# Kernel tuning notes

Hardware: AMD Instinct MI355X
Metric: run time of the kernel (lower is better)

Reference implementation:

```python
import jax, jax.numpy as jnp
import numpy as np

B, A, C, H, W = 4, 5, 64, 128, 128


def _base_grid(h, w):
    # torch F.affine_grid with align_corners=False: pixel-center normalized coords
    xs = (2.0 * jnp.arange(w, dtype=jnp.float32) + 1.0) / w - 1.0
    ys = (2.0 * jnp.arange(h, dtype=jnp.float32) + 1.0) / h - 1.0
    X, Y = jnp.meshgrid(xs, ys)  # [h,w]
    return jnp.stack([X, Y, jnp.ones_like(X)], axis=-1)  # [h,w,3]


def _grid_sample(img, grid):
    # img [C,H,W]; grid [H,W,2] = (x,y) normalized; bilinear, zeros padding, align_corners=False
    c, h, w = img.shape
    ix = ((grid[..., 0] + 1.0) * w - 1.0) * 0.5
    iy = ((grid[..., 1] + 1.0) * h - 1.0) * 0.5
    ix0 = jnp.floor(ix); iy0 = jnp.floor(iy)
    ix1 = ix0 + 1.0; iy1 = iy0 + 1.0
    wx1 = ix - ix0; wy1 = iy - iy0
    wx0 = 1.0 - wx1; wy0 = 1.0 - wy1

    def gather(iyf, ixf):
        valid = (iyf >= 0) & (iyf <= h - 1) & (ixf >= 0) & (ixf <= w - 1)
        iyc = jnp.clip(iyf.astype(jnp.int32), 0, h - 1)
        ixc = jnp.clip(ixf.astype(jnp.int32), 0, w - 1)
        return img[:, iyc, ixc] * valid[None].astype(img.dtype)  # [C,H,W]

    return (gather(iy0, ix0) * (wy0 * wx0)[None]
            + gather(iy0, ix1) * (wy0 * wx1)[None]
            + gather(iy1, ix0) * (wy1 * wx0)[None]
            + gather(iy1, ix1) * (wy1 * wx1)[None])


_sample_batch = jax.vmap(_grid_sample)


def setup_inputs() -> dict:
    key = jax.random.key(0)
    k1, k2, k3 = jax.random.split(key, 3)
    feats = jax.random.normal(k1, (B, A, C, H, W), dtype=jnp.float32)
    trans_matrices = jax.random.normal(k2, (B, A, A, 4, 4), dtype=jnp.float32)
    num_agent_tensor = jax.random.randint(k3, (B, A), 1, A + 1, dtype=jnp.int64)
    return {"feats": feats, "trans_matrices": trans_matrices,
            "num_agent_tensor": num_agent_tensor}


def reference(feats, trans_matrices, num_agent_tensor):
    b, a, c, h, w = feats.shape
    T = trans_matrices  # [B,A(target i),A(neighbor j),4,4]
    zeros = jnp.zeros(T.shape[:3], T.dtype)
    ones = jnp.ones_like(zeros)
    # theta_rot = [[T00, T01, 0], [T10, T11, 0]]
    theta_rot = jnp.stack([
        jnp.stack([T[..., 0, 0], T[..., 0, 1], zeros], axis=-1),
        jnp.stack([T[..., 1, 0], T[..., 1, 1], zeros], axis=-1)], axis=-2)
    x_t = 4.0 * T[..., 0, 3] / 128.0
    y_t = -(4.0 * T[..., 1, 3]) / 128.0
    theta_trans = jnp.stack([
        jnp.stack([ones, zeros, x_t], axis=-1),
        jnp.stack([zeros, ones, y_t], axis=-1)], axis=-2)
    base = _base_grid(h, w)  # [H,W,3]
    grid_rot = jnp.einsum('hwk,bijrk->bijhwr', base, theta_rot)
    grid_trans = jnp.einsum('hwk,bijrk->bijhwr', base, theta_trans)
    n = b * a * a
    # neighbor feature feats[b, j] broadcast over target index i
    feats_nb = jnp.broadcast_to(feats[:, None], (b, a, a, c, h, w)).reshape(n, c, h, w)
    w1 = _sample_batch(feats_nb, grid_rot.reshape(n, h, w, 2))
    w2 = _sample_batch(w1, grid_trans.reshape(n, h, w, 2)).reshape(b, a, a, c, h, w)
    na = num_agent_tensor[:, 0]  # [B]
    ar = jnp.arange(a)
    valid = ((ar[None, :, None] < na[:, None, None])
             & (ar[None, None, :] < na[:, None, None])
             & (ar[:, None] != ar[None, :])[None])  # [B,A_i,A_j]
    fused = feats + jnp.sum(w2 * valid[..., None, None, None].astype(feats.dtype), axis=2)
    # agents2batch: concatenate per-agent slices along batch dim -> [A*B, C, H, W]
    return fused.transpose(1, 0, 2, 3, 4).reshape(a * b, c, h, w)
```

## Files before the change

kernel.cpp:

```cpp
#include <hip/hip_runtime.h>


typedef float floatv4 __attribute__((ext_vector_type(4)));

constexpr int Bc = 4, Ac = 5, Cc = 64, Hc = 128, Wc = 128;
constexpr int HWc = Hc * Wc;
constexpr int NP  = Bc * Ac;
constexpr int NG  = Cc / 4;
constexpr int GPB = 4;
constexpr int TW = 64, TH = 4;
constexpr int WW = TW + 1, WSZ = WW * (TH + 1);
constexpr size_t WS_NEED = (size_t)NP * Cc * HWc * sizeof(float);

__global__ __launch_bounds__(256)
void fafmimo_repack(const float* __restrict__ feats, float4* __restrict__ ws)
{
    const int idx  = (int)(blockIdx.x * 256 + threadIdx.x);
    const int pix4 = (idx & 4095) * 4;
    const int t    = idx >> 12;
    const int g    = t & 15;
    const int p    = t >> 4;
    const floatv4* s =
        (const floatv4*)(feats + ((size_t)p * Cc + g * 4) * HWc + pix4);
    const floatv4 r0 = __builtin_nontemporal_load(s);
    const floatv4 r1 = __builtin_nontemporal_load(s + HWc / 4);
    const floatv4 r2 = __builtin_nontemporal_load(s + 2 * (HWc / 4));
    const floatv4 r3 = __builtin_nontemporal_load(s + 3 * (HWc / 4));
    float4* d = ws + ((size_t)p * NG + g) * HWc + pix4;
    d[0] = make_float4(r0.x, r1.x, r2.x, r3.x);
    d[1] = make_float4(r0.y, r1.y, r2.y, r3.y);
    d[2] = make_float4(r0.z, r1.z, r2.z, r3.z);
    d[3] = make_float4(r0.w, r1.w, r2.w, r3.w);
}

__global__ __launch_bounds__(256)
void fafmimo_main(const float4* __restrict__ ws,
                  const float* __restrict__ trans,
                  const int*   __restrict__ num_agent,
                  float*       __restrict__ out)
{
    __shared__ float4 w1s[GPB][WSZ];

    const int z  = (int)blockIdx.z;
    const int bi = z % NP;
    const int q  = z / NP;
    const int g0 = q * GPB;
    const int b  = bi / Ac;
    const int i  = bi - b * Ac;
    const int tx = (int)threadIdx.x, ty = (int)threadIdx.y;
    const int tid = ty * TW + tx;
    const int x0 = (int)blockIdx.x * TW, y0 = (int)blockIdx.y * TH;
    const int x  = x0 + tx, y = y0 + ty;
    const int pix = y * Wc + x;
    const int na = num_agent[b * Ac];

    const float xv  = (2.0f * (float)x  + 1.0f) / 128.0f - 1.0f;
    const float yv  = (2.0f * (float)y  + 1.0f) / 128.0f - 1.0f;
    const float xv0 = (2.0f * (float)x0 + 1.0f) / 128.0f - 1.0f;
    const float yv0 = (2.0f * (float)y0 + 1.0f) / 128.0f - 1.0f;

    float4 acc[GPB];
    #pragma unroll
    for (int cg = 0; cg < GPB; ++cg)
        acc[cg] = ws[((size_t)bi * NG + g0 + cg) * HWc + pix];

    if (i < na) {
        for (int j = 0; j < Ac; ++j) {
            if (j == i || j >= na) continue;

            const float* Tm = trans + (size_t)((b * Ac + i) * Ac + j) * 16;
            const float r00 = Tm[0], r01 = Tm[1], t03 = Tm[3];
            const float r10 = Tm[4], r11 = Tm[5], t13 = Tm[7];
            const float x_t =  (4.0f * t03) / 128.0f;
            const float y_t = -(4.0f * t13) / 128.0f;

            const int fdx = (int)floorf(((xv0 + x_t + 1.0f) * 128.0f - 1.0f) * 0.5f) - x0;
            const int fdy = (int)floorf(((yv0 + y_t + 1.0f) * 128.0f - 1.0f) * 0.5f) - y0;

            const float4* __restrict__ pj0 = ws + ((size_t)((b * Ac + j) * NG) + g0) * HWc;
            const float4* __restrict__ pj1 = pj0 + HWc;
            const float4* __restrict__ pj2 = pj0 + 2 * HWc;
            const float4* __restrict__ pj3 = pj0 + 3 * HWc;

            for (int e = tid; e < WSZ; e += TW * TH) {
                const int ry = e / WW, rx = e - ry * WW;
                const int jy = y0 + fdy + ry, jx = x0 + fdx + rx;
                const int jyc = min(max(jy, 0), 127);
                const int jxc = min(max(jx, 0), 127);

                const float Xs = (2.0f * (float)jxc + 1.0f) / 128.0f - 1.0f;
                const float Ys = (2.0f * (float)jyc + 1.0f) / 128.0f - 1.0f;
                const float gx = Xs * r00 + Ys * r01;
                const float gy = Xs * r10 + Ys * r11;
                const float ixs = ((gx + 1.0f) * 128.0f - 1.0f) * 0.5f;
                const float iys = ((gy + 1.0f) * 128.0f - 1.0f) * 0.5f;
                const float sx0 = floorf(ixs), sy0 = floorf(iys);
                const float u1 = ixs - sx0, v1 = iys - sy0;
                const float u0 = 1.0f - u1, v0 = 1.0f - v1;

                const bool xin = (sx0 >= 0.0f) & (sx0 <= 126.0f);
                const float a  = xin ? u0 : ((sx0 == -1.0f)  ? u1 : 0.0f);
                const float bb = xin ? u1 : ((sx0 == 127.0f) ? u0 : 0.0f);
                const int xb = min(max((int)sx0, 0), 126);

                const bool vr0 = (sy0 >= 0.0f) & (sy0 <= 127.0f);
                const bool vr1 = (sy0 >= -1.0f) & (sy0 <= 126.0f);
                const float wr0 = v0 * (vr0 ? 1.0f : 0.0f);
                const float wr1 = v1 * (vr1 ? 1.0f : 0.0f);
                const int o0 = min(max((int)sy0, 0), 127) * Wc + xb;
                const int o1 = min(max((int)sy0 + 1, 0), 127) * Wc + xb;

                #pragma unroll
                for (int cg = 0; cg < GPB; ++cg) {
                    const float4* __restrict__ pg =
                        (cg == 0) ? pj0 : (cg == 1) ? pj1 : (cg == 2) ? pj2 : pj3;
                    const float4 t0a = pg[o0], t0b = pg[o0 + 1];
                    const float4 t1a = pg[o1], t1b = pg[o1 + 1];
                    float4 w1;
                    w1.x = wr0 * fmaf(a, t0a.x, bb * t0b.x) + wr1 * fmaf(a, t1a.x, bb * t1b.x);
                    w1.y = wr0 * fmaf(a, t0a.y, bb * t0b.y) + wr1 * fmaf(a, t1a.y, bb * t1b.y);
                    w1.z = wr0 * fmaf(a, t0a.z, bb * t0b.z) + wr1 * fmaf(a, t1a.z, bb * t1b.z);
                    w1.w = wr0 * fmaf(a, t0a.w, bb * t0b.w) + wr1 * fmaf(a, t1a.w, bb * t1b.w);
                    w1s[cg][e] = w1;
                }
            }
            __syncthreads();

            const float ix2 = ((xv + x_t + 1.0f) * 128.0f - 1.0f) * 0.5f;
            const float iy2 = ((yv + y_t + 1.0f) * 128.0f - 1.0f) * 0.5f;
            const int jx0 = x + fdx, jy0 = y + fdy;
            const float fx1 = ix2 - (float)jx0, fx0 = 1.0f - fx1;
            const float fy1 = iy2 - (float)jy0, fy0 = 1.0f - fy1;
            const float vx0 = (jx0 >= 0 && jx0 <= 127) ? 1.0f : 0.0f;
            const float vx1 = (jx0 >= -1 && jx0 <= 126) ? 1.0f : 0.0f;
            const float vy0 = (jy0 >= 0 && jy0 <= 127) ? 1.0f : 0.0f;
            const float vy1 = (jy0 >= -1 && jy0 <= 126) ? 1.0f : 0.0f;
            const float w00 = fy0 * vy0 * fx0 * vx0;
            const float w01 = fy0 * vy0 * fx1 * vx1;
            const float w10 = fy1 * vy1 * fx0 * vx0;
            const float w11 = fy1 * vy1 * fx1 * vx1;

            const int base = ty * WW + tx;
            #pragma unroll
            for (int cg = 0; cg < GPB; ++cg) {
                const float4 s00 = w1s[cg][base],      s01 = w1s[cg][base + 1];
                const float4 s10 = w1s[cg][base + WW], s11 = w1s[cg][base + WW + 1];
                acc[cg].x += w00 * s00.x + w01 * s01.x + w10 * s10.x + w11 * s11.x;
                acc[cg].y += w00 * s00.y + w01 * s01.y + w10 * s10.y + w11 * s11.y;
                acc[cg].z += w00 * s00.z + w01 * s01.z + w10 * s10.z + w11 * s11.z;
                acc[cg].w += w00 * s00.w + w01 * s01.w + w10 * s10.w + w11 * s11.w;
            }
            __syncthreads();
        }
    }

    #pragma unroll
    for (int cg = 0; cg < GPB; ++cg) {
        float* __restrict__ ob =
            out + ((size_t)(i * Bc + b) * Cc + (g0 + cg) * 4) * HWc + pix;
        __builtin_nontemporal_store(acc[cg].x, ob);
        __builtin_nontemporal_store(acc[cg].y, ob + HWc);
        __builtin_nontemporal_store(acc[cg].z, ob + 2 * HWc);
        __builtin_nontemporal_store(acc[cg].w, ob + 3 * HWc);
    }
}

constexpr int CHK = 16;
__global__ __launch_bounds__(256)
void fafmimo_direct(const float* __restrict__ feats,
                    const float* __restrict__ trans,
                    const int*   __restrict__ num_agent,
                    float*       __restrict__ out)
{
    const int z  = (int)blockIdx.z;
    const int bi = z % NP;
    const int c0 = (z / NP) * CHK;
    const int b  = bi / Ac;
    const int i  = bi - b * Ac;
    const int x  = (int)(blockIdx.x * 64 + threadIdx.x);
    const int y  = (int)(blockIdx.y * 4  + threadIdx.y);
    const int pix = y * Wc + x;
    const int na = num_agent[b * Ac];

    const float xv = (2.0f * (float)x + 1.0f) / 128.0f - 1.0f;
    const float yv = (2.0f * (float)y + 1.0f) / 128.0f - 1.0f;

    const float* __restrict__ fi =
        feats + (size_t)(b * Ac + i) * Cc * HWc + (size_t)c0 * HWc;
    float* __restrict__ ob =
        out + (size_t)(i * Bc + b) * Cc * HWc + (size_t)c0 * HWc;

    float acc[CHK];
    #pragma unroll
    for (int k = 0; k < CHK; ++k) acc[k] = fi[k * HWc + pix];

    if (i < na) {
        for (int j = 0; j < Ac; ++j) {
            if (j == i || j >= na) continue;
            const float* Tm = trans + (size_t)((b * Ac + i) * Ac + j) * 16;
            const float r00 = Tm[0], r01 = Tm[1], t03 = Tm[3];
            const float r10 = Tm[4], r11 = Tm[5], t13 = Tm[7];
            const float x_t =  (4.0f * t03) / 128.0f;
            const float y_t = -(4.0f * t13) / 128.0f;
            const float ix2 = ((xv + x_t + 1.0f) * 128.0f - 1.0f) * 0.5f;
            const float iy2 = ((yv + y_t + 1.0f) * 128.0f - 1.0f) * 0.5f;
            const float fx0 = floorf(ix2), fy0 = floorf(iy2);
            const float wx1 = ix2 - fx0,   wy1 = iy2 - fy0;
            const float wx0 = 1.0f - wx1,  wy0 = 1.0f - wy1;

            int off[8]; float wA[8], wB[8];
            #pragma unroll
            for (int cy = 0; cy < 2; ++cy) {
                #pragma unroll
                for (int cx = 0; cx < 2; ++cx) {
                    const float jyf = fy0 + (float)cy;
                    const float jxf = fx0 + (float)cx;
                    const bool v2 = (jyf >= 0.0f) & (jyf <= 127.0f)
                                  & (jxf >= 0.0f) & (jxf <= 127.0f);
                    const float w2 = (cy ? wy1 : wy0) * (cx ? wx1 : wx0)
                                   * (v2 ? 1.0f : 0.0f);
                    const int jy = min(max((int)jyf, 0), 127);
                    const int jx = min(max((int)jxf, 0), 127);
                    const float Xs = (2.0f * (float)jx + 1.0f) / 128.0f - 1.0f;
                    const float Ys = (2.0f * (float)jy + 1.0f) / 128.0f - 1.0f;
                    const float gx = Xs * r00 + Ys * r01;
                    const float gy = Xs * r10 + Ys * r11;
                    const float ixs = ((gx + 1.0f) * 128.0f - 1.0f) * 0.5f;
                    const float iys = ((gy + 1.0f) * 128.0f - 1.0f) * 0.5f;
                    const float sx0 = floorf(ixs), sy0 = floorf(iys);
                    const float u1 = ixs - sx0, v1 = iys - sy0;
                    const float u0 = 1.0f - u1,  v0f = 1.0f - v1;
                    const bool xin = (sx0 >= 0.0f) & (sx0 <= 126.0f);
                    const float a  = xin ? u0 : ((sx0 == -1.0f)  ? u1 : 0.0f);
                    const float bbp = xin ? u1 : ((sx0 == 127.0f) ? u0 : 0.0f);
                    const int xb = min(max((int)sx0, 0), 126);
                    const int e = (cy * 2 + cx) * 2;
                    #pragma unroll
                    for (int r = 0; r < 2; ++r) {
                        const float syr = sy0 + (float)r;
                        const bool vy = (syr >= 0.0f) & (syr <= 127.0f);
                        const float wyr = (r ? v1 : v0f) * (vy ? 1.0f : 0.0f) * w2;
                        const int syc = min(max((int)syr, 0), 127);
                        off[e + r] = syc * Wc + xb;
                        wA[e + r]  = wyr * a;
                        wB[e + r]  = wyr * bbp;
                    }
                }
            }

            const float* __restrict__ fj =
                feats + (size_t)(b * Ac + j) * Cc * HWc + (size_t)c0 * HWc;
            #pragma unroll 4
            for (int k = 0; k < CHK; ++k) {
                const float* __restrict__ p = fj + (size_t)k * HWc;
                float s0 = 0.0f, s1 = 0.0f;
                #pragma unroll
                for (int r = 0; r < 8; ++r) {
                    s0 = fmaf(wA[r], p[off[r]],     s0);
                    s1 = fmaf(wB[r], p[off[r] + 1], s1);
                }
                acc[k] += s0 + s1;
            }
        }
    }

    #pragma unroll
    for (int k = 0; k < CHK; ++k)
        __builtin_nontemporal_store(acc[k], &ob[k * HWc + pix]);
}

extern "C" void kernel_launch(void* const* d_in, const int* in_sizes, int n_in,
                              void* d_out, int out_size, void* d_ws, size_t ws_size,
                              hipStream_t stream) {
    const float* feats     = (const float*)d_in[0];
    const float* trans     = (const float*)d_in[1];
    const int*   num_agent = (const int*)d_in[2];
    float* out = (float*)d_out;

    if (ws_size >= WS_NEED) {
        float4* ws = (float4*)d_ws;
        hipLaunchKernelGGL(fafmimo_repack, dim3(NP * NG * (HWc / 4) / 256),
                           dim3(256), 0, stream, feats, ws);
        dim3 grid(Wc / TW, Hc / TH, NP * (NG / GPB));
        dim3 block(TW, TH, 1);
        hipLaunchKernelGGL(fafmimo_main, grid, block, 0, stream,
                           ws, trans, num_agent, out);
    } else {
        dim3 grid(Wc / 64, Hc / 4, NP * 4);
        dim3 block(64, 4, 1);
        hipLaunchKernelGGL(fafmimo_direct, grid, block, 0, stream,
                           feats, trans, num_agent, out);
    }
}
```

Baseline: 226.2 us.

## Double-buffer shared warp tile across neighbors and halve channel groups per block

Restructures the per-neighbor loop into a double-buffered pipeline. While one shared-memory buffer is being consumed by the second bilinear stencil, the next neighbor's first-stage sample is written into the other buffer, so only one barrier per iteration is needed instead of two. Channel groups per block drop from 4 to 2, which doubles the grid and keeps the shared footprint the same. In exchange, the rotation-stage index math and the trans loads are redone for every block at twice the count, and occupancy depends on the register pressure of the overlapped fill and stencil.

```diff
diff --git a/kernel.cpp b/kernel.cpp
--- a/kernel.cpp
+++ b/kernel.cpp
@@ -7,7 +7,8 @@
 constexpr int HWc = Hc * Wc;
 constexpr int NP  = Bc * Ac;
 constexpr int NG  = Cc / 4;
-constexpr int GPB = 4;
+constexpr int GPB = 2;
+constexpr int NQ  = NG / GPB;
 constexpr int TW = 64, TH = 4;
 constexpr int WW = TW + 1, WSZ = WW * (TH + 1);
 constexpr size_t WS_NEED = (size_t)NP * Cc * HWc * sizeof(float);
@@ -39,12 +40,11 @@
                   const int*   __restrict__ num_agent,
                   float*       __restrict__ out)
 {
-    __shared__ float4 w1s[GPB][WSZ];
+    __shared__ float4 w1s[2][GPB][WSZ];
 
     const int z  = (int)blockIdx.z;
     const int bi = z % NP;
-    const int q  = z / NP;
-    const int g0 = q * GPB;
+    const int g0 = (z / NP) * GPB;
     const int b  = bi / Ac;
     const int i  = bi - b * Ac;
     const int tx = (int)threadIdx.x, ty = (int)threadIdx.y;
@@ -64,93 +64,114 @@
     for (int cg = 0; cg < GPB; ++cg)
         acc[cg] = ws[((size_t)bi * NG + g0 + cg) * HWc + pix];
 
-    if (i < na) {
-        for (int j = 0; j < Ac; ++j) {
-            if (j == i || j >= na) continue;
-
-            const float* Tm = trans + (size_t)((b * Ac + i) * Ac + j) * 16;
-            const float r00 = Tm[0], r01 = Tm[1], t03 = Tm[3];
-            const float r10 = Tm[4], r11 = Tm[5], t13 = Tm[7];
-            const float x_t =  (4.0f * t03) / 128.0f;
-            const float y_t = -(4.0f * t13) / 128.0f;
-
-            const int fdx = (int)floorf(((xv0 + x_t + 1.0f) * 128.0f - 1.0f) * 0.5f) - x0;
-            const int fdy = (int)floorf(((yv0 + y_t + 1.0f) * 128.0f - 1.0f) * 0.5f) - y0;
-
-            const float4* __restrict__ pj0 = ws + ((size_t)((b * Ac + j) * NG) + g0) * HWc;
-            const float4* __restrict__ pj1 = pj0 + HWc;
-            const float4* __restrict__ pj2 = pj0 + 2 * HWc;
-            const float4* __restrict__ pj3 = pj0 + 3 * HWc;
-
-            for (int e = tid; e < WSZ; e += TW * TH) {
-                const int ry = e / WW, rx = e - ry * WW;
-                const int jy = y0 + fdy + ry, jx = x0 + fdx + rx;
-                const int jyc = min(max(jy, 0), 127);
-                const int jxc = min(max(jx, 0), 127);
-
-                const float Xs = (2.0f * (float)jxc + 1.0f) / 128.0f - 1.0f;
-                const float Ys = (2.0f * (float)jyc + 1.0f) / 128.0f - 1.0f;
-                const float gx = Xs * r00 + Ys * r01;
-                const float gy = Xs * r10 + Ys * r11;
-                const float ixs = ((gx + 1.0f) * 128.0f - 1.0f) * 0.5f;
-                const float iys = ((gy + 1.0f) * 128.0f - 1.0f) * 0.5f;
-                const float sx0 = floorf(ixs), sy0 = floorf(iys);
-                const float u1 = ixs - sx0, v1 = iys - sy0;
-                const float u0 = 1.0f - u1, v0 = 1.0f - v1;
-
-                const bool xin = (sx0 >= 0.0f) & (sx0 <= 126.0f);
-                const float a  = xin ? u0 : ((sx0 == -1.0f)  ? u1 : 0.0f);
-                const float bb = xin ? u1 : ((sx0 == 127.0f) ? u0 : 0.0f);
-                const int xb = min(max((int)sx0, 0), 126);
-
-                const bool vr0 = (sy0 >= 0.0f) & (sy0 <= 127.0f);
-                const bool vr1 = (sy0 >= -1.0f) & (sy0 <= 126.0f);
-                const float wr0 = v0 * (vr0 ? 1.0f : 0.0f);
-                const float wr1 = v1 * (vr1 ? 1.0f : 0.0f);
-                const int o0 = min(max((int)sy0, 0), 127) * Wc + xb;
-                const int o1 = min(max((int)sy0 + 1, 0), 127) * Wc + xb;
-
-                #pragma unroll
-                for (int cg = 0; cg < GPB; ++cg) {
-                    const float4* __restrict__ pg =
-                        (cg == 0) ? pj0 : (cg == 1) ? pj1 : (cg == 2) ? pj2 : pj3;
-                    const float4 t0a = pg[o0], t0b = pg[o0 + 1];
-                    const float4 t1a = pg[o1], t1b = pg[o1 + 1];
-                    float4 w1;
-                    w1.x = wr0 * fmaf(a, t0a.x, bb * t0b.x) + wr1 * fmaf(a, t1a.x, bb * t1b.x);
-                    w1.y = wr0 * fmaf(a, t0a.y, bb * t0b.y) + wr1 * fmaf(a, t1a.y, bb * t1b.y);
-                    w1.z = wr0 * fmaf(a, t0a.z, bb * t0b.z) + wr1 * fmaf(a, t1a.z, bb * t1b.z);
-                    w1.w = wr0 * fmaf(a, t0a.w, bb * t0b.w) + wr1 * fmaf(a, t1a.w, bb * t1b.w);
-                    w1s[cg][e] = w1;
-                }
-            }
-            __syncthreads();
-
-            const float ix2 = ((xv + x_t + 1.0f) * 128.0f - 1.0f) * 0.5f;
-            const float iy2 = ((yv + y_t + 1.0f) * 128.0f - 1.0f) * 0.5f;
-            const int jx0 = x + fdx, jy0 = y + fdy;
-            const float fx1 = ix2 - (float)jx0, fx0 = 1.0f - fx1;
-            const float fy1 = iy2 - (float)jy0, fy0 = 1.0f - fy1;
-            const float vx0 = (jx0 >= 0 && jx0 <= 127) ? 1.0f : 0.0f;
-            const float vx1 = (jx0 >= -1 && jx0 <= 126) ? 1.0f : 0.0f;
-            const float vy0 = (jy0 >= 0 && jy0 <= 127) ? 1.0f : 0.0f;
-            const float vy1 = (jy0 >= -1 && jy0 <= 126) ? 1.0f : 0.0f;
-            const float w00 = fy0 * vy0 * fx0 * vx0;
-            const float w01 = fy0 * vy0 * fx1 * vx1;
-            const float w10 = fy1 * vy1 * fx0 * vx0;
-            const float w11 = fy1 * vy1 * fx1 * vx1;
-
-            const int base = ty * WW + tx;
+    auto nextj = [&](int jp) {
+        for (int j = jp + 1; j < na; ++j)
+            if (j != i) return j;
+        return Ac;
+    };
+
+    auto fill = [&](int buf, int j) {
+        const float* Tm = trans + (size_t)((b * Ac + i) * Ac + j) * 16;
+        const float r00 = Tm[0], r01 = Tm[1], t03 = Tm[3];
+        const float r10 = Tm[4], r11 = Tm[5], t13 = Tm[7];
+        const float x_t =  (4.0f * t03) / 128.0f;
+        const float y_t = -(4.0f * t13) / 128.0f;
+        const int fdx = (int)floorf(((xv0 + x_t + 1.0f) * 128.0f - 1.0f) * 0.5f) - x0;
+        const int fdy = (int)floorf(((yv0 + y_t + 1.0f) * 128.0f - 1.0f) * 0.5f) - y0;
+        const float4* __restrict__ pj0 =
+            ws + ((size_t)((b * Ac + j) * NG) + g0) * HWc;
+        const float4* __restrict__ pj1 = pj0 + HWc;
+
+        for (int e = tid; e < WSZ; e += TW * TH) {
+            const int ry = e / WW, rx = e - ry * WW;
+            const int jy = y0 + fdy + ry, jx = x0 + fdx + rx;
+            const int jyc = min(max(jy, 0), 127);
+            const int jxc = min(max(jx, 0), 127);
+
+            const float Xs = (2.0f * (float)jxc + 1.0f) / 128.0f - 1.0f;
+            const float Ys = (2.0f * (float)jyc + 1.0f) / 128.0f - 1.0f;
+            const float gx = Xs * r00 + Ys * r01;
+            const float gy = Xs * r10 + Ys * r11;
+            const float ixs = ((gx + 1.0f) * 128.0f - 1.0f) * 0.5f;
+            const float iys = ((gy + 1.0f) * 128.0f - 1.0f) * 0.5f;
+            const float sx0 = floorf(ixs), sy0 = floorf(iys);
+            const float u1 = ixs - sx0, v1 = iys - sy0;
+            const float u0 = 1.0f - u1, v0 = 1.0f - v1;
+
+            const bool xin = (sx0 >= 0.0f) & (sx0 <= 126.0f);
+            const float a  = xin ? u0 : ((sx0 == -1.0f)  ? u1 : 0.0f);
+            const float bb = xin ? u1 : ((sx0 == 127.0f) ? u0 : 0.0f);
+            const int xb = min(max((int)sx0, 0), 126);
+
+            const bool vr0 = (sy0 >= 0.0f) & (sy0 <= 127.0f);
+            const bool vr1 = (sy0 >= -1.0f) & (sy0 <= 126.0f);
+            const float wr0 = v0 * (vr0 ? 1.0f : 0.0f);
+            const float wr1 = v1 * (vr1 ? 1.0f : 0.0f);
+            const int o0 = min(max((int)sy0, 0), 127) * Wc + xb;
+            const int o1 = min(max((int)sy0 + 1, 0), 127) * Wc + xb;
+
             #pragma unroll
             for (int cg = 0; cg < GPB; ++cg) {
-                const float4 s00 = w1s[cg][base],      s01 = w1s[cg][base + 1];
-                const float4 s10 = w1s[cg][base + WW], s11 = w1s[cg][base + WW + 1];
-                acc[cg].x += w00 * s00.x + w01 * s01.x + w10 * s10.x + w11 * s11.x;
-                acc[cg].y += w00 * s00.y + w01 * s01.y + w10 * s10.y + w11 * s11.y;
-                acc[cg].z += w00 * s00.z + w01 * s01.z + w10 * s10.z + w11 * s11.z;
-                acc[cg].w += w00 * s00.w + w01 * s01.w + w10 * s10.w + w11 * s11.w;
+                const float4* __restrict__ pg = (cg == 0) ? pj0 : pj1;
+                const float4 t0a = pg[o0], t0b = pg[o0 + 1];
+                const float4 t1a = pg[o1], t1b = pg[o1 + 1];
+                float4 w1;
+                w1.x = wr0 * fmaf(a, t0a.x, bb * t0b.x) + wr1 * fmaf(a, t1a.x, bb * t1b.x);
+                w1.y = wr0 * fmaf(a, t0a.y, bb * t0b.y) + wr1 * fmaf(a, t1a.y, bb * t1b.y);
+                w1.z = wr0 * fmaf(a, t0a.z, bb * t0b.z) + wr1 * fmaf(a, t1a.z, bb * t1b.z);
+                w1.w = wr0 * fmaf(a, t0a.w, bb * t0b.w) + wr1 * fmaf(a, t1a.w, bb * t1b.w);
+                w1s[buf][cg][e] = w1;
             }
-            __syncthreads();
+        }
+    };
+
+    auto stencil = [&](int buf, int j) {
+        const float* Tm = trans + (size_t)((b * Ac + i) * Ac + j) * 16;
+        const float t03 = Tm[3], t13 = Tm[7];
+        const float x_t =  (4.0f * t03) / 128.0f;
+        const float y_t = -(4.0f * t13) / 128.0f;
+        const int fdx = (int)floorf(((xv0 + x_t + 1.0f) * 128.0f - 1.0f) * 0.5f) - x0;
+        const int fdy = (int)floorf(((yv0 + y_t + 1.0f) * 128.0f - 1.0f) * 0.5f) - y0;
+
+        const float ix2 = ((xv + x_t + 1.0f) * 128.0f - 1.0f) * 0.5f;
+        const float iy2 = ((yv + y_t + 1.0f) * 128.0f - 1.0f) * 0.5f;
+        const int jx0 = x + fdx, jy0 = y + fdy;
+        const float fx1 = ix2 - (float)jx0, fx0 = 1.0f - fx1;
+        const float fy1 = iy2 - (float)jy0, fy0 = 1.0f - fy1;
+        const float vx0 = (jx0 >= 0 && jx0 <= 127) ? 1.0f : 0.0f;
+        const float vx1 = (jx0 >= -1 && jx0 <= 126) ? 1.0f : 0.0f;
+        const float vy0 = (jy0 >= 0 && jy0 <= 127) ? 1.0f : 0.0f;
+        const float vy1 = (jy0 >= -1 && jy0 <= 126) ? 1.0f : 0.0f;
+        const float w00 = fy0 * vy0 * fx0 * vx0;
+        const float w01 = fy0 * vy0 * fx1 * vx1;
+        const float w10 = fy1 * vy1 * fx0 * vx0;
+        const float w11 = fy1 * vy1 * fx1 * vx1;
+
+        const int base = ty * WW + tx;
+        #pragma unroll
+        for (int cg = 0; cg < GPB; ++cg) {
+            const float4 s00 = w1s[buf][cg][base],      s01 = w1s[buf][cg][base + 1];
+            const float4 s10 = w1s[buf][cg][base + WW], s11 = w1s[buf][cg][base + WW + 1];
+            acc[cg].x += w00 * s00.x + w01 * s01.x + w10 * s10.x + w11 * s11.x;
+            acc[cg].y += w00 * s00.y + w01 * s01.y + w10 * s10.y + w11 * s11.y;
+            acc[cg].z += w00 * s00.z + w01 * s01.z + w10 * s10.z + w11 * s11.z;
+            acc[cg].w += w00 * s00.w + w01 * s01.w + w10 * s10.w + w11 * s11.w;
+        }
+    };
+
+    if (i < na) {
+        int jc = nextj(-1);
+        if (jc < Ac) {
+            fill(0, jc);
+            int cur = 0;
+            while (true) {
+                const int jn = nextj(jc);
+                __syncthreads();
+                if (jn < Ac) fill(cur ^ 1, jn);
+                stencil(cur, jc);
+                if (jn >= Ac) break;
+                jc = jn; cur ^= 1;
+            }
         }
     }
 
@@ -281,7 +302,7 @@
         float4* ws = (float4*)d_ws;
         hipLaunchKernelGGL(fafmimo_repack, dim3(NP * NG * (HWc / 4) / 256),
                            dim3(256), 0, stream, feats, ws);
-        dim3 grid(Wc / TW, Hc / TH, NP * (NG / GPB));
+        dim3 grid(Wc / TW, Hc / TH, NP * NQ);
         dim3 block(TW, TH, 1);
         hipLaunchKernelGGL(fafmimo_main, grid, block, 0, stream,
                            ws, trans, num_agent, out);
```

Result: faster. 217.6 us (-3.8%).
